# Optimization experiments

Measured on AMD Instinct MI355X. Metric: run time of the kernel, lower is better.

Reference implementation:

```python
import jax, jax.numpy as jnp
import numpy as np

SLOPE = 25.0  # snntorch fast_sigmoid default slope
ALPHA = 1.0   # gradient-reversal strength (forward default)

@jax.custom_vjp
def fs_spike(x):
    return (x > 0).astype(x.dtype)
def _fs_fwd(x):
    return (x > 0).astype(x.dtype), x
def _fs_bwd(x, g):
    return (g / (SLOPE * jnp.abs(x) + 1.0) ** 2,)
fs_spike.defvjp(_fs_fwd, _fs_bwd)

@jax.custom_vjp
def atan_spike(x):  # snntorch default ATan surrogate (alpha=2)
    return (x > 0).astype(x.dtype)
def _at_fwd(x):
    return (x > 0).astype(x.dtype), x
def _at_bwd(x, g):
    return (g / (1.0 + (jnp.pi * x) ** 2),)
atan_spike.defvjp(_at_fwd, _at_bwd)

@jax.custom_vjp
def grad_reverse(x):
    return x
def _gr_fwd(x):
    return x, None
def _gr_bwd(_, g):
    return (-ALPHA * g,)
grad_reverse.defvjp(_gr_fwd, _gr_bwd)

def lstm_cell(x, h, c, w_ih, w_hh, b_ih, b_hh):
    gates = x @ w_ih.T + b_ih + h @ w_hh.T + b_hh
    i, f, g, o = jnp.split(gates, 4, axis=-1)
    c_new = jax.nn.sigmoid(f) * c + jax.nn.sigmoid(i) * jnp.tanh(g)
    h_new = jax.nn.sigmoid(o) * jnp.tanh(c_new)
    return h_new, c_new

def slstm_step(x, syn, mem, w_ih, w_hh, b_ih, b_hh, thr):
    # reset computed from previous mem, detached (snntorch mem_reset)
    reset = jax.lax.stop_gradient((mem - thr > 0).astype(mem.dtype))
    h, c = lstm_cell(x, mem, syn, w_ih, w_hh, b_ih, b_hh)
    mem_new = h - reset * thr  # reset_mechanism='subtract'
    spk = fs_spike(mem_new - thr)
    return spk, c, mem_new

def _forward(x, conv_w, bn_gamma, bn_beta, thr_lif1,
             w_ih1, w_hh1, b_ih1, b_hh1, thr1,
             w_ih2, w_hh2, b_ih2, b_hh2, thr2,
             fc_g_w, fc_g_b, fc_d1_w, fc_d1_b, thr_dom, fc_d2_w, fc_d2_b):
    T, B, C = x.shape
    xc = jnp.transpose(x, (1, 2, 0))  # [B, C, T]
    conv = jax.lax.conv_general_dilated(xc, conv_w, window_strides=(1,),
                                        padding=[(2, 2)],
                                        dimension_numbers=('NCH', 'OIH', 'NCH'))
    # BatchNorm1d in training mode: batch stats over (B, T) per channel
    mu = conv.mean(axis=(0, 2), keepdims=True)
    var = conv.var(axis=(0, 2), keepdims=True)
    bn = (conv - mu) / jnp.sqrt(var + 1e-5) * bn_gamma[None, :, None] + bn_beta[None, :, None]
    # Leaky neuron, single step from zero mem: mem = input, spk = fire(mem - thr)
    spk_conv = atan_spike(bn - thr_lif1)
    seq = jnp.transpose(spk_conv, (2, 0, 1))  # [T, B, 64]
    H = w_hh1.shape[1]
    init = (jnp.zeros((B, H), x.dtype), jnp.zeros((B, H), x.dtype),
            jnp.zeros((B, H), x.dtype), jnp.zeros((B, H), x.dtype))

    def step(carry, xt):
        syn1, mem1, syn2, mem2 = carry
        spk1, syn1, mem1 = slstm_step(xt, syn1, mem1, w_ih1, w_hh1, b_ih1, b_hh1, thr1)
        spk2, syn2, mem2 = slstm_step(spk1, syn2, mem2, w_ih2, w_hh2, b_ih2, b_hh2, thr2)
        return (syn1, mem1, syn2, mem2), mem2

    _, mem2_rec = jax.lax.scan(step, init, seq)  # [T, B, H]
    features = mem2_rec.mean(axis=0)             # [B, H]
    gesture = features @ fc_g_w.T + fc_g_b
    rev = grad_reverse(features)
    domain_hidden = atan_spike(rev @ fc_d1_w.T + fc_d1_b - thr_dom)
    domain = domain_hidden @ fc_d2_w.T + fc_d2_b
    return gesture, domain

def setup_inputs() -> dict:
    key = jax.random.key(0)
    ks = jax.random.split(key, 16)
    T, B, C, H = 2000, 256, 14, 128
    f = jnp.float32
    return {
        'x': jax.random.normal(ks[0], (T, B, C), f),
        'conv_w': jax.random.normal(ks[1], (64, C, 5), f) * 0.12,
        'bn_gamma': jnp.ones((64,), f),
        'bn_beta': jnp.zeros((64,), f),
        'thr_lif1': jnp.ones((), f),
        'w_ih1': jax.random.normal(ks[2], (4 * H, 64), f) * 0.08,
        'w_hh1': jax.random.normal(ks[3], (4 * H, H), f) * 0.08,
        'b_ih1': jnp.zeros((4 * H,), f),
        'b_hh1': jnp.zeros((4 * H,), f),
        'thr1': jnp.ones((), f),
        'w_ih2': jax.random.normal(ks[4], (4 * H, H), f) * 0.08,
        'w_hh2': jax.random.normal(ks[5], (4 * H, H), f) * 0.08,
        'b_ih2': jnp.zeros((4 * H,), f),
        'b_hh2': jnp.zeros((4 * H,), f),
        'thr2': jnp.ones((), f),
        'fc_g_w': jax.random.normal(ks[6], (8, H), f) * 0.08,
        'fc_g_b': jnp.zeros((8,), f),
        'fc_d1_w': jax.random.normal(ks[7], (64, H), f) * 0.08,
        'fc_d1_b': jnp.zeros((64,), f),
        'thr_dom': jnp.ones((), f),
        'fc_d2_w': jax.random.normal(ks[8], (10, 64), f) * 0.1,
        'fc_d2_b': jnp.zeros((10,), f),
    }

def reference(x, conv_w, bn_gamma, bn_beta, thr_lif1,
              w_ih1, w_hh1, b_ih1, b_hh1, thr1,
              w_ih2, w_hh2, b_ih2, b_hh2, thr2,
              fc_g_w, fc_g_b, fc_d1_w, fc_d1_b, thr_dom, fc_d2_w, fc_d2_b):
    return _forward(x, conv_w, bn_gamma, bn_beta, thr_lif1,
                    w_ih1, w_hh1, b_ih1, b_hh1, thr1,
                    w_ih2, w_hh2, b_ih2, b_hh2, thr2,
                    fc_g_w, fc_g_b, fc_d1_w, fc_d1_b, thr_dom, fc_d2_w, fc_d2_b)
```

## Files before the change

kernel.cpp:

```cpp
#include <hip/hip_runtime.h>
#include <cstdint>
#include <cstddef>

#define TSTEPS 2000
#define NB     256
#define HID    128
#define CIN    14
#define NGRP   64
#define RG     4
#define BPG    4

#define OFF_CNT   0ull
#define OFF_M1WS  8192ull
#define OFF_M2WS  (OFF_M1WS + 262144ull)
#define OFF_SPKW  (OFF_M2WS + 262144ull)
#define OFF_FEAT  (OFF_SPKW + 8192ull)
#define OFF_AB    (OFF_FEAT + 131072ull)
#define OFF_PART  (OFF_AB   + 512ull)
#define OFF_MASK  (OFF_PART + 1179648ull)
#define ZERO_WORDS 133120

__global__ __launch_bounds__(256) void k0_zero(unsigned* ws) {
  int i = blockIdx.x * 256 + threadIdx.x;
  if (i < ZERO_WORDS) ws[i] = 0u;
}

__global__ __launch_bounds__(256) void k1_stats(const float* __restrict__ x,
                                                const float* __restrict__ cw,
                                                float* __restrict__ part) {
  __shared__ float xLds[244 * CIN];
  __shared__ float cwLds[64 * 70];
  __shared__ float red[2][4][64];
  const int b = blockIdx.x, tile = blockIdx.y;
  const int base = tile * 240;
  for (int f = threadIdx.x; f < 244 * CIN; f += 256) {
    int u = f / CIN, ci = f - u * CIN;
    int tp = base + u - 2;
    xLds[f] = (tp >= 0 && tp < TSTEPS) ? x[((size_t)tp * NB + b) * CIN + ci] : 0.0f;
  }
  for (int f = threadIdx.x; f < 64 * 70; f += 256) cwLds[f] = cw[f];
  __syncthreads();

  const int co = threadIdx.x & 63, tq = threadIdx.x >> 6;
  float cwr[70];
#pragma unroll
  for (int s = 0; s < 70; ++s) cwr[s] = cwLds[co * 70 + s];
  float xw[5][CIN];
  const int u0 = tq * 60;
#pragma unroll
  for (int r = 0; r < 4; ++r)
#pragma unroll
    for (int ci = 0; ci < CIN; ++ci) xw[r][ci] = xLds[(u0 + r) * CIN + ci];

  float s1 = 0.0f, s2 = 0.0f;
  const int tbase = base + tq * 60;
  for (int i5 = 0; i5 < 60; i5 += 5) {
#pragma unroll
    for (int s = 0; s < 5; ++s) {
#pragma unroll
      for (int ci = 0; ci < CIN; ++ci)
        xw[(s + 4) % 5][ci] = xLds[(u0 + i5 + s + 4) * CIN + ci];
      float y = 0.0f;
#pragma unroll
      for (int kk = 0; kk < 5; ++kk)
#pragma unroll
        for (int ci = 0; ci < CIN; ++ci)
          y += xw[(s + kk) % 5][ci] * cwr[ci * 5 + kk];
      if (tbase + i5 + s < TSTEPS) { s1 += y; s2 += y * y; }
    }
  }
  red[0][tq][co] = s1; red[1][tq][co] = s2;
  __syncthreads();
  if (threadIdx.x < 64) {
    float a1 = red[0][0][co] + red[0][1][co] + red[0][2][co] + red[0][3][co];
    float a2 = red[1][0][co] + red[1][1][co] + red[1][2][co] + red[1][3][co];
    int blk = tile * NB + b;
    part[blk * 128 + co * 2 + 0] = a1;
    part[blk * 128 + co * 2 + 1] = a2;
  }
}

__global__ __launch_bounds__(256) void k1b_reduce(const float* __restrict__ gamma,
                           const float* __restrict__ beta,
                           const float* __restrict__ part, float* __restrict__ ab) {
  __shared__ float red[2][4][64];
  const int co = threadIdx.x & 63, pt = threadIdx.x >> 6;
  float s1 = 0.0f, s2 = 0.0f;
  for (int blk = pt * 576; blk < pt * 576 + 576; ++blk) {
    s1 += part[blk * 128 + co * 2 + 0];
    s2 += part[blk * 128 + co * 2 + 1];
  }
  red[0][pt][co] = s1; red[1][pt][co] = s2;
  __syncthreads();
  if (threadIdx.x < 64) {
    float a1 = red[0][0][co] + red[0][1][co] + red[0][2][co] + red[0][3][co];
    float a2 = red[1][0][co] + red[1][1][co] + red[1][2][co] + red[1][3][co];
    const float N = (float)TSTEPS * (float)NB;
    float mu = a1 / N;
    float var = a2 / N - mu * mu;
    float rstd = 1.0f / sqrtf(var + 1e-5f);
    float a = gamma[co] * rstd;
    ab[co] = a;
    ab[64 + co] = beta[co] - mu * a;
  }
}

__global__ __launch_bounds__(256) void k2_spike(const float* __restrict__ x,
                                                const float* __restrict__ cw,
                                                const float* __restrict__ thrp,
                                                const float* __restrict__ ab,
                                                unsigned long long* __restrict__ masks) {
  __shared__ float xLds[244 * CIN];
  __shared__ float cwLds[64 * 70];
  const int b = blockIdx.x, tile = blockIdx.y;
  const int base = tile * 240;
  for (int f = threadIdx.x; f < 244 * CIN; f += 256) {
    int u = f / CIN, ci = f - u * CIN;
    int tp = base + u - 2;
    xLds[f] = (tp >= 0 && tp < TSTEPS) ? x[((size_t)tp * NB + b) * CIN + ci] : 0.0f;
  }
  for (int f = threadIdx.x; f < 64 * 70; f += 256) cwLds[f] = cw[f];
  __syncthreads();

  const int co = threadIdx.x & 63, tq = threadIdx.x >> 6;
  const float thr = thrp[0];
  const float aC = ab[co], bC = ab[64 + co];
  float cwr[70];
#pragma unroll
  for (int s = 0; s < 70; ++s) cwr[s] = cwLds[co * 70 + s];
  float xw[5][CIN];
  const int u0 = tq * 60;
#pragma unroll
  for (int r = 0; r < 4; ++r)
#pragma unroll
    for (int ci = 0; ci < CIN; ++ci) xw[r][ci] = xLds[(u0 + r) * CIN + ci];

  const int tbase = base + tq * 60;
  for (int i5 = 0; i5 < 60; i5 += 5) {
#pragma unroll
    for (int s = 0; s < 5; ++s) {
#pragma unroll
      for (int ci = 0; ci < CIN; ++ci)
        xw[(s + 4) % 5][ci] = xLds[(u0 + i5 + s + 4) * CIN + ci];
      float y = 0.0f;
#pragma unroll
      for (int kk = 0; kk < 5; ++kk)
#pragma unroll
        for (int ci = 0; ci < CIN; ++ci)
          y += xw[(s + kk) % 5][ci] * cwr[ci * 5 + kk];
      int t = tbase + i5 + s;
      if (t < TSTEPS) {
        float bn = y * aC + bC;
        unsigned long long m = __ballot(bn - thr > 0.0f);
        if (co == 0) masks[(size_t)t * NB + b] = m;
      }
    }
  }
}

__global__ __launch_bounds__(512, 2) void kp_fused(char* ws,
    const float* __restrict__ w_ih1, const float* __restrict__ w_hh1,
    const float* __restrict__ b_ih1, const float* __restrict__ b_hh1,
    const float* __restrict__ thr1p,
    const float* __restrict__ w_ih2, const float* __restrict__ w_hh2,
    const float* __restrict__ b_ih2, const float* __restrict__ b_hh2,
    const float* __restrict__ thr2p) {
  __shared__ __align__(16) float A1[192 * 4];
  __shared__ __align__(16) float A2[256 * 4];
  __shared__ float gateL[128 * 5];
  __shared__ float biasL1[128], biasL2[128];

  const int tid = threadIdx.x;
  const int bid = blockIdx.x;
  const int g = bid & 63;
  const int q = bid >> 6;
  const int lane = tid & 63, wv = tid >> 6;
  const int idx = lane & 15, kq = lane >> 4;
  const int a = idx & 3, hlq = idx >> 2;
  const int hl = hlq * 8 + wv;
  const int j = a * 32 + hl;
  const int grow = a * 128 + q * 32 + hl;

  unsigned* cnt = (unsigned*)(ws + OFF_CNT) + g * 32;
  float* m1ws = (float*)(ws + OFF_M1WS);
  float* m2ws = (float*)(ws + OFF_M2WS);
  unsigned* spkw = (unsigned*)(ws + OFF_SPKW);
  float* feat = (float*)(ws + OFF_FEAT);
  const unsigned long long* masks = (const unsigned long long*)(ws + OFF_MASK);

  float wr1[48];
#pragma unroll
  for (int i = 0; i < 48; ++i) {
    int k = ((i >> 1) << 3) + (kq << 1) + (i & 1);
    wr1[i] = (k < 64) ? w_ih1[grow * 64 + k] : w_hh1[grow * 128 + (k - 64)];
  }
  float wr2[64];
#pragma unroll
  for (int i = 0; i < 64; ++i) {
    int k = ((i >> 1) << 3) + (kq << 1) + (i & 1);
    wr2[i] = (k < 128) ? w_ih2[grow * 128 + k] : w_hh2[grow * 128 + (k - 128)];
  }
  if (tid < 128) {
    int aa = tid >> 5, h2 = tid & 31;
    int gr = aa * 128 + q * 32 + h2;
    biasL1[tid] = b_ih1[gr] + b_hh1[gr];
    biasL2[tid] = b_ih2[gr] + b_hh2[gr];
  }
  const float thr1 = thr1p[0], thr2 = thr2p[0];
  const int cr = tid >> 5, chl = tid & 31;
  float syn1 = 0.0f, mem1 = 0.0f, syn2 = 0.0f, mem2 = 0.0f, facc = 0.0f;
  __syncthreads();

  unsigned long long mrow = masks[(size_t)0 * NB + g * RG + (tid & 3)];

  for (int p = 0; p < TSTEPS; ++p) {
    {
      int f = tid;
#pragma unroll
      for (int pass = 0; pass < 2; ++pass, f += 512) {
        if (f < 768) {
          int k = f >> 2, e = f & 3;
          float v;
          if (k < 64) v = (float)((mrow >> k) & 1ull);
          else v = __hip_atomic_load(
                     &m1ws[((((p + 1) & 1) * 64 + g) * 4 + e) * 128 + (k - 64)],
                     __ATOMIC_RELAXED, __HIP_MEMORY_SCOPE_AGENT);
          A1[f] = v;
        }
      }
    }
    __syncthreads();

    float ac0 = 0.0f, ac1 = 0.0f, ac2 = 0.0f, ac3 = 0.0f;
    {
      const float* Ab = A1 + (kq << 3);
#pragma unroll
      for (int m = 0; m < 24; ++m) {
#pragma unroll
        for (int b2 = 0; b2 < 2; ++b2) {
          float4 av = *(const float4*)(Ab + m * 32 + b2 * 4);
          float w = wr1[m * 2 + b2];
          ac0 += w * av.x; ac1 += w * av.y; ac2 += w * av.z; ac3 += w * av.w;
        }
      }
    }
    ac0 += __shfl_xor(ac0, 16); ac1 += __shfl_xor(ac1, 16);
    ac2 += __shfl_xor(ac2, 16); ac3 += __shfl_xor(ac3, 16);
    ac0 += __shfl_xor(ac0, 32); ac1 += __shfl_xor(ac1, 32);
    ac2 += __shfl_xor(ac2, 32); ac3 += __shfl_xor(ac3, 32);
    if (kq == 0) {
      gateL[j * 5 + 0] = ac0; gateL[j * 5 + 1] = ac1;
      gateL[j * 5 + 2] = ac2; gateL[j * 5 + 3] = ac3;
    }
    __syncthreads();

    if (tid < 128) {
      float g0 = biasL1[chl]       + gateL[(chl) * 5 + cr];
      float g1 = biasL1[32 + chl]  + gateL[(32 + chl) * 5 + cr];
      float g2 = biasL1[64 + chl]  + gateL[(64 + chl) * 5 + cr];
      float g3 = biasL1[96 + chl]  + gateL[(96 + chl) * 5 + cr];
      float rst = (mem1 - thr1 > 0.0f) ? thr1 : 0.0f;
      float ig = 1.0f / (1.0f + expf(-g0));
      float fg = 1.0f / (1.0f + expf(-g1));
      float gg = tanhf(g2);
      float og = 1.0f / (1.0f + expf(-g3));
      float cn = fg * syn1 + ig * gg;
      float mn = og * tanhf(cn) - rst;
      syn1 = cn; mem1 = mn;
      __hip_atomic_store(&m1ws[(((p & 1) * 64 + g) * 4 + cr) * 128 + (q * 32 + chl)],
                         mn, __ATOMIC_RELAXED, __HIP_MEMORY_SCOPE_AGENT);
      unsigned long long bal = __ballot(mn - thr1 > 0.0f);
      if (lane == 0)
        __hip_atomic_store(&spkw[(((p & 1) * 64 + g) * 4 + (wv * 2 + 0)) * 4 + q],
                           (unsigned)(bal & 0xffffffffull),
                           __ATOMIC_RELAXED, __HIP_MEMORY_SCOPE_AGENT);
      if (lane == 32)
        __hip_atomic_store(&spkw[(((p & 1) * 64 + g) * 4 + (wv * 2 + 1)) * 4 + q],
                           (unsigned)(bal >> 32),
                           __ATOMIC_RELAXED, __HIP_MEMORY_SCOPE_AGENT);
    }
    __syncthreads();

    if (tid == 0) {
      atomicAdd(cnt, 1u);
      const unsigned tgt = 4u * (unsigned)(p + 1);
      while (__hip_atomic_load(cnt, __ATOMIC_RELAXED, __HIP_MEMORY_SCOPE_AGENT) < tgt)
        __builtin_amdgcn_s_sleep(1);
    }
    __syncthreads();

    if (p + 1 < TSTEPS) mrow = masks[(size_t)(p + 1) * NB + g * RG + (tid & 3)];
    {
      int f = tid;
#pragma unroll
      for (int pass = 0; pass < 2; ++pass, f += 512) {
        int k = f >> 2, e = f & 3;
        float v;
        if (k < 128) {
          unsigned u = __hip_atomic_load(
              &spkw[(((p & 1) * 64 + g) * 4 + e) * 4 + (k >> 5)],
              __ATOMIC_RELAXED, __HIP_MEMORY_SCOPE_AGENT);
          v = (float)((u >> (k & 31)) & 1u);
        } else {
          v = __hip_atomic_load(
              &m2ws[((((p + 1) & 1) * 64 + g) * 4 + e) * 128 + (k - 128)],
              __ATOMIC_RELAXED, __HIP_MEMORY_SCOPE_AGENT);
        }
        A2[f] = v;
      }
    }
    __syncthreads();

    ac0 = 0.0f; ac1 = 0.0f; ac2 = 0.0f; ac3 = 0.0f;
    {
      const float* Ab = A2 + (kq << 3);
#pragma unroll
      for (int m = 0; m < 32; ++m) {
#pragma unroll
        for (int b2 = 0; b2 < 2; ++b2) {
          float4 av = *(const float4*)(Ab + m * 32 + b2 * 4);
          float w = wr2[m * 2 + b2];
          ac0 += w * av.x; ac1 += w * av.y; ac2 += w * av.z; ac3 += w * av.w;
        }
      }
    }
    ac0 += __shfl_xor(ac0, 16); ac1 += __shfl_xor(ac1, 16);
    ac2 += __shfl_xor(ac2, 16); ac3 += __shfl_xor(ac3, 16);
    ac0 += __shfl_xor(ac0, 32); ac1 += __shfl_xor(ac1, 32);
    ac2 += __shfl_xor(ac2, 32); ac3 += __shfl_xor(ac3, 32);
    if (kq == 0) {
      gateL[j * 5 + 0] = ac0; gateL[j * 5 + 1] = ac1;
      gateL[j * 5 + 2] = ac2; gateL[j * 5 + 3] = ac3;
    }
    __syncthreads();

    if (tid < 128) {
      float g0 = biasL2[chl]       + gateL[(chl) * 5 + cr];
      float g1 = biasL2[32 + chl]  + gateL[(32 + chl) * 5 + cr];
      float g2 = biasL2[64 + chl]  + gateL[(64 + chl) * 5 + cr];
      float g3 = biasL2[96 + chl]  + gateL[(96 + chl) * 5 + cr];
      float rst = (mem2 - thr2 > 0.0f) ? thr2 : 0.0f;
      float ig = 1.0f / (1.0f + expf(-g0));
      float fg = 1.0f / (1.0f + expf(-g1));
      float gg = tanhf(g2);
      float og = 1.0f / (1.0f + expf(-g3));
      float cn = fg * syn2 + ig * gg;
      float mn = og * tanhf(cn) - rst;
      syn2 = cn; mem2 = mn;
      __hip_atomic_store(&m2ws[(((p & 1) * 64 + g) * 4 + cr) * 128 + (q * 32 + chl)],
                         mn, __ATOMIC_RELAXED, __HIP_MEMORY_SCOPE_AGENT);
      facc += mn;
    }
  }

  if (tid < 128)
    feat[(g * RG + cr) * 128 + q * 32 + chl] = facc * (1.0f / (float)TSTEPS);
}

__global__ __launch_bounds__(128) void k3_head(const float* __restrict__ feat,
    const float* __restrict__ gw, const float* __restrict__ gb,
    const float* __restrict__ d1w, const float* __restrict__ d1b,
    const float* __restrict__ thrdp,
    const float* __restrict__ d2w, const float* __restrict__ d2b,
    float* __restrict__ out) {
  __shared__ float fL[128];
  __shared__ float dh[64];
  const int b = blockIdx.x, t = threadIdx.x;
  fL[t] = feat[b * 128 + t];
  __syncthreads();
  if (t < 64) {
    float s = d1b[t];
    for (int k = 0; k < 128; ++k) s += d1w[t * 128 + k] * fL[k];
    dh[t] = (s - thrdp[0] > 0.0f) ? 1.0f : 0.0f;
  }
  __syncthreads();
  if (t < 8) {
    float s = gb[t];
    for (int k = 0; k < 128; ++k) s += gw[t * 128 + k] * fL[k];
    out[b * 8 + t] = s;
  }
  if (t >= 64 && t < 74) {
    const int o = t - 64;
    float s = d2b[o];
    for (int k = 0; k < 64; ++k) s += d2w[o * 64 + k] * dh[k];
    out[2048 + b * 10 + o] = s;
  }
}

extern "C" void kernel_launch(void* const* d_in, const int* in_sizes, int n_in,
                              void* d_out, int out_size, void* d_ws, size_t ws_size,
                              hipStream_t stream) {
  const float* x      = (const float*)d_in[0];
  const float* conv_w = (const float*)d_in[1];
  const float* bn_g   = (const float*)d_in[2];
  const float* bn_b   = (const float*)d_in[3];
  const float* thrl1  = (const float*)d_in[4];
  const float* w_ih1  = (const float*)d_in[5];
  const float* w_hh1  = (const float*)d_in[6];
  const float* b_ih1  = (const float*)d_in[7];
  const float* b_hh1  = (const float*)d_in[8];
  const float* thr1   = (const float*)d_in[9];
  const float* w_ih2  = (const float*)d_in[10];
  const float* w_hh2  = (const float*)d_in[11];
  const float* b_ih2  = (const float*)d_in[12];
  const float* b_hh2  = (const float*)d_in[13];
  const float* thr2   = (const float*)d_in[14];
  const float* fc_g_w = (const float*)d_in[15];
  const float* fc_g_b = (const float*)d_in[16];
  const float* fc_d1w = (const float*)d_in[17];
  const float* fc_d1b = (const float*)d_in[18];
  const float* thrdom = (const float*)d_in[19];
  const float* fc_d2w = (const float*)d_in[20];
  const float* fc_d2b = (const float*)d_in[21];
  float* out = (float*)d_out;
  char* ws = (char*)d_ws;

  k0_zero<<<(ZERO_WORDS + 255) / 256, 256, 0, stream>>>((unsigned*)ws);
  k1_stats<<<dim3(NB, 9), 256, 0, stream>>>(x, conv_w, (float*)(ws + OFF_PART));
  k1b_reduce<<<1, 256, 0, stream>>>(bn_g, bn_b, (const float*)(ws + OFF_PART),
                                    (float*)(ws + OFF_AB));
  k2_spike<<<dim3(NB, 9), 256, 0, stream>>>(x, conv_w, thrl1,
                                            (const float*)(ws + OFF_AB),
                                            (unsigned long long*)(ws + OFF_MASK));
  kp_fused<<<NGRP * BPG, 512, 0, stream>>>(ws, w_ih1, w_hh1, b_ih1, b_hh1, thr1,
                                           w_ih2, w_hh2, b_ih2, b_hh2, thr2);
  k3_head<<<NB, 128, 0, stream>>>((const float*)(ws + OFF_FEAT), fc_g_w, fc_g_b,
                                  fc_d1w, fc_d1b, thrdom, fc_d2w, fc_d2b, out);
}
```

Baseline: 17.68 ms.

## Skew the two LSTM layers into one phase with a single grid barrier per step

Software-pipelines the two recurrent layers so that at step p layer 1 computes step p while layer 2 computes step p-1, both from state published in the previous iteration. This halves the shared-memory sync phases and removes one of the two cross-block waits per timestep. The atomic counter barrier becomes per-block flag stores that four threads poll, and launch bounds drop the min-blocks hint. In exchange it adds an extra loop iteration, a second gate buffer, and more delicate double-buffer index bookkeeping that must stay race-free.

```diff
diff --git a/kernel.cpp b/kernel.cpp
--- a/kernel.cpp
+++ b/kernel.cpp
@@ -158,7 +158,7 @@
   }
 }
 
-__global__ __launch_bounds__(512, 2) void kp_fused(char* ws,
+__global__ __launch_bounds__(512) void kp_fused(char* ws,
     const float* __restrict__ w_ih1, const float* __restrict__ w_hh1,
     const float* __restrict__ b_ih1, const float* __restrict__ b_hh1,
     const float* __restrict__ thr1p,
@@ -167,7 +167,8 @@
     const float* __restrict__ thr2p) {
   __shared__ __align__(16) float A1[192 * 4];
   __shared__ __align__(16) float A2[256 * 4];
-  __shared__ float gateL[128 * 5];
+  __shared__ float gate1L[128 * 5];
+  __shared__ float gate2L[128 * 5];
   __shared__ float biasL1[128], biasL2[128];
 
   const int tid = threadIdx.x;
@@ -181,7 +182,7 @@
   const int j = a * 32 + hl;
   const int grow = a * 128 + q * 32 + hl;
 
-  unsigned* cnt = (unsigned*)(ws + OFF_CNT) + g * 32;
+  unsigned* flags = (unsigned*)(ws + OFF_CNT);
   float* m1ws = (float*)(ws + OFF_M1WS);
   float* m2ws = (float*)(ws + OFF_M2WS);
   unsigned* spkw = (unsigned*)(ws + OFF_SPKW);
@@ -213,26 +214,45 @@
 
   unsigned long long mrow = masks[(size_t)0 * NB + g * RG + (tid & 3)];
 
-  for (int p = 0; p < TSTEPS; ++p) {
-    {
-      int f = tid;
-#pragma unroll
-      for (int pass = 0; pass < 2; ++pass, f += 512) {
-        if (f < 768) {
-          int k = f >> 2, e = f & 3;
-          float v;
-          if (k < 64) v = (float)((mrow >> k) & 1ull);
-          else v = __hip_atomic_load(
-                     &m1ws[((((p + 1) & 1) * 64 + g) * 4 + e) * 128 + (k - 64)],
-                     __ATOMIC_RELAXED, __HIP_MEMORY_SCOPE_AGENT);
-          A1[f] = v;
-        }
-      }
-    }
+  for (int p = 0; p <= TSTEPS; ++p) {
+    const int rb1 = (p + 1) & 1;
+    const int wb = p & 1;
+
+    {
+      int k = tid >> 2, e = tid & 3;
+      float v;
+      if (k < 64) v = (float)((mrow >> k) & 1ull);
+      else v = __hip_atomic_load(&m1ws[((rb1 * 64 + g) * 4 + e) * 128 + (k - 64)],
+                                 __ATOMIC_RELAXED, __HIP_MEMORY_SCOPE_AGENT);
+      A1[tid] = v;
+    }
+    {
+      int f = tid + 512;
+      if (f < 768) {
+        int k = f >> 2, e = f & 3;
+        float v = __hip_atomic_load(&m1ws[((rb1 * 64 + g) * 4 + e) * 128 + (k - 64)],
+                                    __ATOMIC_RELAXED, __HIP_MEMORY_SCOPE_AGENT);
+        A1[f] = v;
+      }
+    }
+    {
+      int k = tid >> 2, e = tid & 3;
+      unsigned u = __hip_atomic_load(&spkw[((rb1 * 64 + g) * 4 + e) * 4 + (k >> 5)],
+                                     __ATOMIC_RELAXED, __HIP_MEMORY_SCOPE_AGENT);
+      A2[tid] = (float)((u >> (k & 31)) & 1u);
+    }
+    {
+      int f = tid + 512;
+      int k = f >> 2, e = f & 3;
+      float v = __hip_atomic_load(&m2ws[((wb * 64 + g) * 4 + e) * 128 + (k - 128)],
+                                  __ATOMIC_RELAXED, __HIP_MEMORY_SCOPE_AGENT);
+      A2[f] = v;
+    }
+    if (p + 1 < TSTEPS) mrow = masks[(size_t)(p + 1) * NB + g * RG + (tid & 3)];
     __syncthreads();
 
-    float ac0 = 0.0f, ac1 = 0.0f, ac2 = 0.0f, ac3 = 0.0f;
-    {
+    {
+      float ac0 = 0.0f, ac1 = 0.0f, ac2 = 0.0f, ac3 = 0.0f;
       const float* Ab = A1 + (kq << 3);
 #pragma unroll
       for (int m = 0; m < 24; ++m) {
@@ -243,22 +263,43 @@
           ac0 += w * av.x; ac1 += w * av.y; ac2 += w * av.z; ac3 += w * av.w;
         }
       }
-    }
-    ac0 += __shfl_xor(ac0, 16); ac1 += __shfl_xor(ac1, 16);
-    ac2 += __shfl_xor(ac2, 16); ac3 += __shfl_xor(ac3, 16);
-    ac0 += __shfl_xor(ac0, 32); ac1 += __shfl_xor(ac1, 32);
-    ac2 += __shfl_xor(ac2, 32); ac3 += __shfl_xor(ac3, 32);
-    if (kq == 0) {
-      gateL[j * 5 + 0] = ac0; gateL[j * 5 + 1] = ac1;
-      gateL[j * 5 + 2] = ac2; gateL[j * 5 + 3] = ac3;
+      ac0 += __shfl_xor(ac0, 16); ac1 += __shfl_xor(ac1, 16);
+      ac2 += __shfl_xor(ac2, 16); ac3 += __shfl_xor(ac3, 16);
+      ac0 += __shfl_xor(ac0, 32); ac1 += __shfl_xor(ac1, 32);
+      ac2 += __shfl_xor(ac2, 32); ac3 += __shfl_xor(ac3, 32);
+      if (kq == 0) {
+        gate1L[j * 5 + 0] = ac0; gate1L[j * 5 + 1] = ac1;
+        gate1L[j * 5 + 2] = ac2; gate1L[j * 5 + 3] = ac3;
+      }
+    }
+    {
+      float ac0 = 0.0f, ac1 = 0.0f, ac2 = 0.0f, ac3 = 0.0f;
+      const float* Ab = A2 + (kq << 3);
+#pragma unroll
+      for (int m = 0; m < 32; ++m) {
+#pragma unroll
+        for (int b2 = 0; b2 < 2; ++b2) {
+          float4 av = *(const float4*)(Ab + m * 32 + b2 * 4);
+          float w = wr2[m * 2 + b2];
+          ac0 += w * av.x; ac1 += w * av.y; ac2 += w * av.z; ac3 += w * av.w;
+        }
+      }
+      ac0 += __shfl_xor(ac0, 16); ac1 += __shfl_xor(ac1, 16);
+      ac2 += __shfl_xor(ac2, 16); ac3 += __shfl_xor(ac3, 16);
+      ac0 += __shfl_xor(ac0, 32); ac1 += __shfl_xor(ac1, 32);
+      ac2 += __shfl_xor(ac2, 32); ac3 += __shfl_xor(ac3, 32);
+      if (kq == 0) {
+        gate2L[j * 5 + 0] = ac0; gate2L[j * 5 + 1] = ac1;
+        gate2L[j * 5 + 2] = ac2; gate2L[j * 5 + 3] = ac3;
+      }
     }
     __syncthreads();
 
-    if (tid < 128) {
-      float g0 = biasL1[chl]       + gateL[(chl) * 5 + cr];
-      float g1 = biasL1[32 + chl]  + gateL[(32 + chl) * 5 + cr];
-      float g2 = biasL1[64 + chl]  + gateL[(64 + chl) * 5 + cr];
-      float g3 = biasL1[96 + chl]  + gateL[(96 + chl) * 5 + cr];
+    if (tid < 128 && p < TSTEPS) {
+      float g0 = biasL1[chl]       + gate1L[(chl) * 5 + cr];
+      float g1 = biasL1[32 + chl]  + gate1L[(32 + chl) * 5 + cr];
+      float g2 = biasL1[64 + chl]  + gate1L[(64 + chl) * 5 + cr];
+      float g3 = biasL1[96 + chl]  + gate1L[(96 + chl) * 5 + cr];
       float rst = (mem1 - thr1 > 0.0f) ? thr1 : 0.0f;
       float ig = 1.0f / (1.0f + expf(-g0));
       float fg = 1.0f / (1.0f + expf(-g1));
@@ -267,78 +308,23 @@
       float cn = fg * syn1 + ig * gg;
       float mn = og * tanhf(cn) - rst;
       syn1 = cn; mem1 = mn;
-      __hip_atomic_store(&m1ws[(((p & 1) * 64 + g) * 4 + cr) * 128 + (q * 32 + chl)],
+      __hip_atomic_store(&m1ws[((wb * 64 + g) * 4 + cr) * 128 + (q * 32 + chl)],
                          mn, __ATOMIC_RELAXED, __HIP_MEMORY_SCOPE_AGENT);
       unsigned long long bal = __ballot(mn - thr1 > 0.0f);
       if (lane == 0)
-        __hip_atomic_store(&spkw[(((p & 1) * 64 + g) * 4 + (wv * 2 + 0)) * 4 + q],
+        __hip_atomic_store(&spkw[((wb * 64 + g) * 4 + (wv * 2 + 0)) * 4 + q],
                            (unsigned)(bal & 0xffffffffull),
                            __ATOMIC_RELAXED, __HIP_MEMORY_SCOPE_AGENT);
       if (lane == 32)
-        __hip_atomic_store(&spkw[(((p & 1) * 64 + g) * 4 + (wv * 2 + 1)) * 4 + q],
+        __hip_atomic_store(&spkw[((wb * 64 + g) * 4 + (wv * 2 + 1)) * 4 + q],
                            (unsigned)(bal >> 32),
                            __ATOMIC_RELAXED, __HIP_MEMORY_SCOPE_AGENT);
     }
-    __syncthreads();
-
-    if (tid == 0) {
-      atomicAdd(cnt, 1u);
-      const unsigned tgt = 4u * (unsigned)(p + 1);
-      while (__hip_atomic_load(cnt, __ATOMIC_RELAXED, __HIP_MEMORY_SCOPE_AGENT) < tgt)
-        __builtin_amdgcn_s_sleep(1);
-    }
-    __syncthreads();
-
-    if (p + 1 < TSTEPS) mrow = masks[(size_t)(p + 1) * NB + g * RG + (tid & 3)];
-    {
-      int f = tid;
-#pragma unroll
-      for (int pass = 0; pass < 2; ++pass, f += 512) {
-        int k = f >> 2, e = f & 3;
-        float v;
-        if (k < 128) {
-          unsigned u = __hip_atomic_load(
-              &spkw[(((p & 1) * 64 + g) * 4 + e) * 4 + (k >> 5)],
-              __ATOMIC_RELAXED, __HIP_MEMORY_SCOPE_AGENT);
-          v = (float)((u >> (k & 31)) & 1u);
-        } else {
-          v = __hip_atomic_load(
-              &m2ws[((((p + 1) & 1) * 64 + g) * 4 + e) * 128 + (k - 128)],
-              __ATOMIC_RELAXED, __HIP_MEMORY_SCOPE_AGENT);
-        }
-        A2[f] = v;
-      }
-    }
-    __syncthreads();
-
-    ac0 = 0.0f; ac1 = 0.0f; ac2 = 0.0f; ac3 = 0.0f;
-    {
-      const float* Ab = A2 + (kq << 3);
-#pragma unroll
-      for (int m = 0; m < 32; ++m) {
-#pragma unroll
-        for (int b2 = 0; b2 < 2; ++b2) {
-          float4 av = *(const float4*)(Ab + m * 32 + b2 * 4);
-          float w = wr2[m * 2 + b2];
-          ac0 += w * av.x; ac1 += w * av.y; ac2 += w * av.z; ac3 += w * av.w;
-        }
-      }
-    }
-    ac0 += __shfl_xor(ac0, 16); ac1 += __shfl_xor(ac1, 16);
-    ac2 += __shfl_xor(ac2, 16); ac3 += __shfl_xor(ac3, 16);
-    ac0 += __shfl_xor(ac0, 32); ac1 += __shfl_xor(ac1, 32);
-    ac2 += __shfl_xor(ac2, 32); ac3 += __shfl_xor(ac3, 32);
-    if (kq == 0) {
-      gateL[j * 5 + 0] = ac0; gateL[j * 5 + 1] = ac1;
-      gateL[j * 5 + 2] = ac2; gateL[j * 5 + 3] = ac3;
-    }
-    __syncthreads();
-
-    if (tid < 128) {
-      float g0 = biasL2[chl]       + gateL[(chl) * 5 + cr];
-      float g1 = biasL2[32 + chl]  + gateL[(32 + chl) * 5 + cr];
-      float g2 = biasL2[64 + chl]  + gateL[(64 + chl) * 5 + cr];
-      float g3 = biasL2[96 + chl]  + gateL[(96 + chl) * 5 + cr];
+    if (tid < 128 && p >= 1) {
+      float g0 = biasL2[chl]       + gate2L[(chl) * 5 + cr];
+      float g1 = biasL2[32 + chl]  + gate2L[(32 + chl) * 5 + cr];
+      float g2 = biasL2[64 + chl]  + gate2L[(64 + chl) * 5 + cr];
+      float g3 = biasL2[96 + chl]  + gate2L[(96 + chl) * 5 + cr];
       float rst = (mem2 - thr2 > 0.0f) ? thr2 : 0.0f;
       float ig = 1.0f / (1.0f + expf(-g0));
       float fg = 1.0f / (1.0f + expf(-g1));
@@ -347,9 +333,23 @@
       float cn = fg * syn2 + ig * gg;
       float mn = og * tanhf(cn) - rst;
       syn2 = cn; mem2 = mn;
-      __hip_atomic_store(&m2ws[(((p & 1) * 64 + g) * 4 + cr) * 128 + (q * 32 + chl)],
+      __hip_atomic_store(&m2ws[((rb1 * 64 + g) * 4 + cr) * 128 + (q * 32 + chl)],
                          mn, __ATOMIC_RELAXED, __HIP_MEMORY_SCOPE_AGENT);
       facc += mn;
+    }
+    __syncthreads();
+
+    if (p < TSTEPS) {
+      if (tid == 0)
+        __hip_atomic_store(&flags[(g * 4 + q) * 8], (unsigned)(p + 1),
+                           __ATOMIC_RELAXED, __HIP_MEMORY_SCOPE_AGENT);
+      if (tid < 4) {
+        while (__hip_atomic_load(&flags[(g * 4 + tid) * 8],
+                                 __ATOMIC_RELAXED, __HIP_MEMORY_SCOPE_AGENT)
+               < (unsigned)(p + 1))
+          __builtin_amdgcn_s_sleep(1);
+      }
+      __syncthreads();
     }
   }
 
```

Measured after the change: 17.46 ms. No clear change (-1.3%).
